# Kernel tuning notes

Hardware: AMD Instinct MI355X
Metric: run time of the kernel (lower is better)

The kernel has to match this reference:

```python
import jax, jax.numpy as jnp
import numpy as np

B, S, D = 2, 1024, 1024
H = 4 * D          # SwiGLU hidden
E = 8              # routed experts
K = 2              # top_k
NS = 1             # shared experts


def setup_inputs() -> dict:
    key = jax.random.key(0)
    ks = jax.random.split(key, 8)
    sc = 0.02  # init scale for stability
    return {
        "x": jax.random.normal(ks[0], (B, S, D), jnp.float32),
        "shared_w1": jax.random.normal(ks[1], (NS, D, H), jnp.float32) * sc,
        "shared_w2": jax.random.normal(ks[2], (NS, D, H), jnp.float32) * sc,
        "shared_w3": jax.random.normal(ks[3], (NS, H, D), jnp.float32) * sc,
        "w1": jax.random.normal(ks[4], (E, D, H), jnp.float32) * sc,
        "w2": jax.random.normal(ks[5], (E, D, H), jnp.float32) * sc,
        "w3": jax.random.normal(ks[6], (E, H, D), jnp.float32) * sc,
        "router_w": jax.random.normal(ks[7], (E, D), jnp.float32) * sc,
    }


def _experts(xf, W1, W2, W3):
    # xf: [T, D]; W1,W2: [E, D, H]; W3: [E, H, D] -> [E, T, D]
    h = jax.nn.silu(jnp.einsum("td,edh->eth", xf, W1)) * jnp.einsum("td,edh->eth", xf, W2)
    return jnp.einsum("eth,ehd->etd", h, W3)


def reference(x, shared_w1, shared_w2, shared_w3, w1, w2, w3, router_w):
    b, s, d = x.shape
    xf = x.reshape(-1, d)                       # [T, D]
    T = xf.shape[0]

    # shared experts (summed over NS experts)
    shared_out = _experts(xf, shared_w1, shared_w2, shared_w3).sum(axis=0)  # [T, D]

    # router: nn.Linear(dim, E, bias=False) => x @ W^T
    logits = jnp.einsum("td,ed->te", xf, router_w)   # [T, E]
    probs = jax.nn.softmax(logits, axis=1)
    topw, topi = jax.lax.top_k(probs, K)             # [T, K]
    topw = topw / topw.sum(axis=-1, keepdims=True)

    # dense combine-weight matrix [T, E]: zero except at selected experts
    cw = jnp.zeros((T, E), x.dtype).at[jnp.arange(T)[:, None], topi].add(topw)

    # all-expert outputs, weighted combine (faithful to masked loop + scatter-add)
    y = _experts(xf, w1, w2, w3)                     # [E, T, D]
    routed = jnp.einsum("te,etd->td", cw, y)         # [T, D]

    out = (shared_out + routed).reshape(b, s, d)
    return (out, logits)
```

## Files before the change

### kernel.cpp

```cpp
#include <hip/hip_runtime.h>


#define TD 2048
#define DD 1024
#define HH 4096
#define NEXP 8

typedef _Float16 f16x8 __attribute__((ext_vector_type(8)));
typedef _Float16 f16x4 __attribute__((ext_vector_type(4)));
typedef float f32x4 __attribute__((ext_vector_type(4)));

#define WS_COUNTS   0
#define WS_CURS     64
#define WS_HBASE    128
#define WS_TOKLIST  256
#define WS_TOPI     65792
#define WS_TOPW     82176
#define WS_POS      98560
#define WS_XH       131072
#define WS_H        4325376
#define WS_WT       63045632
#define WTSLOT      ((size_t)DD * HH)

typedef __attribute__((address_space(3))) void lds_void;
typedef const __attribute__((address_space(1))) void gbl_void;
__device__ __forceinline__ void gld16(void* l, const void* g) {
  __builtin_amdgcn_global_load_lds((gbl_void*)g, (lds_void*)l, 16, 0, 0);
}

__device__ __forceinline__ f16x8 frag_ld(const _Float16* tile, int r, int qsel) {
  int q = qsel ^ ((r >> 1) & 3);
  return *(const f16x8*)((const char*)tile + r * 64 + q * 16);
}

__global__ __launch_bounds__(256) void k_xh(const float* __restrict__ x, _Float16* __restrict__ xh) {
  int i = (blockIdx.x * 256 + threadIdx.x) * 8;
  float4 a = *(const float4*)(x + i), b = *(const float4*)(x + i + 4);
  f16x8 v = {(_Float16)a.x, (_Float16)a.y, (_Float16)a.z, (_Float16)a.w,
             (_Float16)b.x, (_Float16)b.y, (_Float16)b.z, (_Float16)b.w};
  *(f16x8*)(xh + i) = v;
}

__global__ __launch_bounds__(256) void k_router(const float* __restrict__ x,
    const float* __restrict__ rw, float* __restrict__ logits,
    int* __restrict__ topi, float* __restrict__ topw, int* __restrict__ counts) {
  int wv = threadIdx.x >> 6, lane = threadIdx.x & 63;
  int t = blockIdx.x * 4 + wv;
  const float* xt = x + (size_t)t * DD;
  float lg[NEXP];
#pragma unroll
  for (int e = 0; e < NEXP; ++e) {
    const float* we = rw + e * DD;
    float acc = 0.f;
#pragma unroll
    for (int j = 0; j < DD / 64; ++j) acc += xt[j * 64 + lane] * we[j * 64 + lane];
#pragma unroll
    for (int off = 32; off; off >>= 1) acc += __shfl_xor(acc, off);
    lg[e] = acc;
  }
  if (lane == 0) {
    float m = lg[0];
#pragma unroll
    for (int e = 1; e < NEXP; ++e) m = fmaxf(m, lg[e]);
    float p[NEXP];
#pragma unroll
    for (int e = 0; e < NEXP; ++e) p[e] = __expf(lg[e] - m);
    int i0 = 0; float p0 = p[0];
#pragma unroll
    for (int e = 1; e < NEXP; ++e) if (p[e] > p0) { p0 = p[e]; i0 = e; }
    int i1 = -1; float p1 = -1.f;
#pragma unroll
    for (int e = 0; e < NEXP; ++e) if (e != i0 && p[e] > p1) { p1 = p[e]; i1 = e; }
    float wsum = p0 + p1;
#pragma unroll
    for (int e = 0; e < NEXP; ++e) logits[t * NEXP + e] = lg[e];
    topi[t * 2] = i0; topi[t * 2 + 1] = i1;
    topw[t * 2] = p0 / wsum; topw[t * 2 + 1] = p1 / wsum;
    atomicAdd(&counts[i0], 1); atomicAdd(&counts[i1], 1);
  }
}

__global__ void k_offsets(const int* __restrict__ counts, int* __restrict__ hbase) {
  if (threadIdx.x == 0) {
    int base = TD;
    for (int e = 0; e < NEXP; ++e) { hbase[e] = base; base += (counts[e] + 127) & ~127; }
  }
}

__global__ void k_scatter(const int* __restrict__ topi, int* __restrict__ curs,
                          int* __restrict__ tokl, int* __restrict__ posarr) {
  int tid = blockIdx.x * 256 + threadIdx.x;
  if (tid >= TD * 2) return;
  int e = topi[tid];
  int pos = atomicAdd(&curs[e], 1);
  tokl[e * TD + pos] = tid >> 1;
  posarr[tid] = pos;
}

__device__ __forceinline__ void transpose_tile(const float* __restrict__ src,
    _Float16* __restrict__ dst, int R, int C, int r0, int c0) {
  __shared__ _Float16 tile[64][68];
  int t = threadIdx.x;
#pragma unroll
  for (int i = 0; i < 4; ++i) {
    int r = (t >> 4) + i * 16;
    int c = (t & 15) * 4;
    float4 v = *(const float4*)(src + (size_t)(r0 + r) * C + c0 + c);
    *(f16x4*)&tile[r][c] = (f16x4){(_Float16)v.x, (_Float16)v.y, (_Float16)v.z, (_Float16)v.w};
  }
  __syncthreads();
#pragma unroll
  for (int i = 0; i < 2; ++i) {
    int cc = (t >> 3) + i * 32;
    int rr = (t & 7) * 8;
    f16x8 hv;
#pragma unroll
    for (int j = 0; j < 8; ++j) hv[j] = tile[rr + j][cc];
    *(f16x8*)(dst + (size_t)(c0 + cc) * R + r0 + rr) = hv;
  }
}

__global__ __launch_bounds__(256) void k_tr1(const float* __restrict__ sw1, const float* __restrict__ sw2,
    const float* __restrict__ w1, const float* __restrict__ w2, _Float16* __restrict__ wt) {
  int id = blockIdx.y;
  const float* src = (id == 0) ? sw1 : (id == 1) ? sw2
                   : (id < 10) ? w1 + (size_t)(id - 2) * DD * HH
                               : w2 + (size_t)(id - 10) * DD * HH;
  _Float16* dst = wt + (size_t)id * WTSLOT;
  transpose_tile(src, dst, DD, HH, (blockIdx.x >> 6) * 64, (blockIdx.x & 63) * 64);
}

__global__ __launch_bounds__(256) void k_tr2(const float* __restrict__ sw3,
    const float* __restrict__ w3, _Float16* __restrict__ wt) {
  int id = blockIdx.y;
  const float* src = (id == 0) ? sw3 : w3 + (size_t)(id - 1) * HH * DD;
  _Float16* dst = wt + (size_t)id * WTSLOT;
  transpose_tile(src, dst, HH, DD, (blockIdx.x >> 4) * 64, (blockIdx.x & 15) * 64);
}

__global__ __launch_bounds__(256, 2) void k_gemm1(
    const _Float16* __restrict__ xh, const _Float16* __restrict__ wt,
    const int* __restrict__ counts, const int* __restrict__ hbase,
    const int* __restrict__ tok_list, _Float16* __restrict__ h) {
  __shared__ _Float16 lA[128 * 32];
  __shared__ _Float16 lB1[128 * 32];
  __shared__ _Float16 lB2[128 * 32];
  __shared__ int stok[128];

  int slot = blockIdx.y;
  const _Float16 *w1t, *w2t;
  int hrow0;
  if (slot < 16) {
    w1t = wt; w2t = wt + WTSLOT; hrow0 = slot * 128;
  } else {
    int e = (slot - 16) >> 4, rt = (slot - 16) & 15;
    if (rt * 128 >= counts[e]) return;
    w1t = wt + (size_t)(2 + e) * WTSLOT;
    w2t = wt + (size_t)(10 + e) * WTSLOT;
    hrow0 = hbase[e] + rt * 128;
  }
  if (threadIdx.x < 128) {
    int tok = (slot < 16) ? (hrow0 + threadIdx.x)
                          : tok_list[((slot - 16) >> 4) * TD + ((slot - 16) & 15) * 128 + threadIdx.x];
    stok[threadIdx.x] = tok;
  }
  __syncthreads();

  int n0 = blockIdx.x * 128;
  int wv = threadIdx.x >> 6, lane = threadIdx.x & 63;
  int wm = (wv & 1) * 64, wn = (wv >> 1) * 64;
  int qsel = lane >> 4;

  const _Float16 *gA[2], *gB1[2], *gB2[2];
  int ldsoff[2];
#pragma unroll
  for (int jj = 0; jj < 2; ++jj) {
    int j = wv * 2 + jj;
    int n = j * 16 + (lane >> 2);
    int q = (lane & 3) ^ ((n >> 1) & 3);
    gA[jj]  = xh + (size_t)stok[n] * DD + q * 8;
    gB1[jj] = w1t + (size_t)(n0 + n) * DD + q * 8;
    gB2[jj] = w2t + (size_t)(n0 + n) * DD + q * 8;
    ldsoff[jj] = j * 1024 + lane * 16;
  }

  f32x4 acc1[4][4] = {}; f32x4 acc2[4][4] = {};

  for (int kk = 0; kk < DD; kk += 32) {
    __syncthreads();
#pragma unroll
    for (int jj = 0; jj < 2; ++jj) {
      gld16((char*)lA + ldsoff[jj], gA[jj] + kk);
      gld16((char*)lB1 + ldsoff[jj], gB1[jj] + kk);
      gld16((char*)lB2 + ldsoff[jj], gB2[jj] + kk);
    }
    __syncthreads();
    f16x8 af[4];
#pragma unroll
    for (int mi = 0; mi < 4; ++mi) af[mi] = frag_ld(lA, wm + mi * 16 + (lane & 15), qsel);
#pragma unroll
    for (int ni = 0; ni < 4; ++ni) {
      f16x8 b1 = frag_ld(lB1, wn + ni * 16 + (lane & 15), qsel);
      f16x8 b2 = frag_ld(lB2, wn + ni * 16 + (lane & 15), qsel);
#pragma unroll
      for (int mi = 0; mi < 4; ++mi) {
        acc1[mi][ni] = __builtin_amdgcn_mfma_f32_16x16x32_f16(af[mi], b1, acc1[mi][ni], 0, 0, 0);
        acc2[mi][ni] = __builtin_amdgcn_mfma_f32_16x16x32_f16(af[mi], b2, acc2[mi][ni], 0, 0, 0);
      }
    }
  }
#pragma unroll
  for (int mi = 0; mi < 4; ++mi)
#pragma unroll
    for (int ni = 0; ni < 4; ++ni)
#pragma unroll
      for (int i = 0; i < 4; ++i) {
        int r = wm + mi * 16 + (lane >> 4) * 4 + i;
        int c = wn + ni * 16 + (lane & 15);
        float a = acc1[mi][ni][i], b = acc2[mi][ni][i];
        h[(size_t)(hrow0 + r) * HH + n0 + c] = (_Float16)((a / (1.f + __expf(-a))) * b);
      }
}

__global__ __launch_bounds__(256, 2) void k_gemm2(
    const _Float16* __restrict__ h, const _Float16* __restrict__ wt,
    const int* __restrict__ counts, const int* __restrict__ hbase,
    _Float16* __restrict__ y0, _Float16* __restrict__ y1) {
  __shared__ _Float16 lA[128 * 32];
  __shared__ _Float16 lB[128 * 32];

  int slot = blockIdx.y;
  const _Float16* w3t;
  int hrow0;
  if (slot < 16) {
    w3t = wt; hrow0 = slot * 128;
  } else {
    int e = (slot - 16) >> 4, rt = (slot - 16) & 15;
    if (rt * 128 >= counts[e]) return;
    w3t = wt + (size_t)(1 + e) * WTSLOT;
    hrow0 = hbase[e] + rt * 128;
  }
  _Float16* y = blockIdx.z ? y1 : y0;
  int kz0 = blockIdx.z * (HH / 2);

  int n0 = blockIdx.x * 128;
  int wv = threadIdx.x >> 6, lane = threadIdx.x & 63;
  int wm = (wv & 1) * 64, wn = (wv >> 1) * 64;
  int qsel = lane >> 4;

  const _Float16 *gA[2], *gB[2];
  int ldsoff[2];
#pragma unroll
  for (int jj = 0; jj < 2; ++jj) {
    int j = wv * 2 + jj;
    int n = j * 16 + (lane >> 2);
    int q = (lane & 3) ^ ((n >> 1) & 3);
    gA[jj] = h   + (size_t)(hrow0 + n) * HH + kz0 + q * 8;
    gB[jj] = w3t + (size_t)(n0 + n)   * HH + kz0 + q * 8;
    ldsoff[jj] = j * 1024 + lane * 16;
  }

  f32x4 acc[4][4] = {};
  for (int kk = 0; kk < HH / 2; kk += 32) {
    __syncthreads();
#pragma unroll
    for (int jj = 0; jj < 2; ++jj) {
      gld16((char*)lA + ldsoff[jj], gA[jj] + kk);
      gld16((char*)lB + ldsoff[jj], gB[jj] + kk);
    }
    __syncthreads();
    f16x8 af[4];
#pragma unroll
    for (int mi = 0; mi < 4; ++mi) af[mi] = frag_ld(lA, wm + mi * 16 + (lane & 15), qsel);
#pragma unroll
    for (int ni = 0; ni < 4; ++ni) {
      f16x8 bf = frag_ld(lB, wn + ni * 16 + (lane & 15), qsel);
#pragma unroll
      for (int mi = 0; mi < 4; ++mi)
        acc[mi][ni] = __builtin_amdgcn_mfma_f32_16x16x32_f16(af[mi], bf, acc[mi][ni], 0, 0, 0);
    }
  }
#pragma unroll
  for (int mi = 0; mi < 4; ++mi)
#pragma unroll
    for (int ni = 0; ni < 4; ++ni)
#pragma unroll
      for (int i = 0; i < 4; ++i) {
        int r = wm + mi * 16 + (lane >> 4) * 4 + i;
        int c = wn + ni * 16 + (lane & 15);
        y[(size_t)(hrow0 + r) * DD + n0 + c] = (_Float16)acc[mi][ni][i];
      }
}

__global__ __launch_bounds__(256) void k_combine(
    const _Float16* __restrict__ y0, const _Float16* __restrict__ y1,
    const int* __restrict__ topi, const float* __restrict__ topw,
    const int* __restrict__ posarr, const int* __restrict__ hbase,
    float* __restrict__ out) {
  int t = blockIdx.x;
  int c = threadIdx.x * 4;
  int e0 = topi[2 * t], e1 = topi[2 * t + 1];
  float w0 = topw[2 * t], w1 = topw[2 * t + 1];
  size_t rs = (size_t)t * DD + c;
  size_t r0 = (size_t)(hbase[e0] + posarr[2 * t]) * DD + c;
  size_t r1 = (size_t)(hbase[e1] + posarr[2 * t + 1]) * DD + c;
  f16x4 s0 = *(const f16x4*)(y0 + rs), s1 = *(const f16x4*)(y1 + rs);
  f16x4 a0 = *(const f16x4*)(y0 + r0), a1 = *(const f16x4*)(y1 + r0);
  f16x4 b0 = *(const f16x4*)(y0 + r1), b1 = *(const f16x4*)(y1 + r1);
  float4 o;
  float* op = &o.x;
#pragma unroll
  for (int i = 0; i < 4; ++i)
    op[i] = (float)s0[i] + (float)s1[i] + w0 * ((float)a0[i] + (float)a1[i])
          + w1 * ((float)b0[i] + (float)b1[i]);
  *(float4*)(out + rs) = o;
}

extern "C" void kernel_launch(void* const* d_in, const int* in_sizes, int n_in,
                              void* d_out, int out_size, void* d_ws, size_t ws_size,
                              hipStream_t stream) {
  const float* x   = (const float*)d_in[0];
  const float* sw1 = (const float*)d_in[1];
  const float* sw2 = (const float*)d_in[2];
  const float* sw3 = (const float*)d_in[3];
  const float* w1  = (const float*)d_in[4];
  const float* w2  = (const float*)d_in[5];
  const float* w3  = (const float*)d_in[6];
  const float* rw  = (const float*)d_in[7];
  float* out = (float*)d_out;
  char* ws = (char*)d_ws;

  int*   counts = (int*)(ws + WS_COUNTS);
  int*   curs   = (int*)(ws + WS_CURS);
  int*   hbase  = (int*)(ws + WS_HBASE);
  int*   tokl   = (int*)(ws + WS_TOKLIST);
  int*   topi   = (int*)(ws + WS_TOPI);
  float* topw   = (float*)(ws + WS_TOPW);
  int*   posarr = (int*)(ws + WS_POS);
  _Float16* xh   = (_Float16*)(ws + WS_XH);
  _Float16* hbuf = (_Float16*)(ws + WS_H);
  _Float16* wt   = (_Float16*)(ws + WS_WT);
  _Float16* ybuf0 = wt + 9 * WTSLOT;
  _Float16* ybuf1 = wt + 11 * WTSLOT;

  hipMemsetAsync(ws, 0, 65792, stream);

  k_xh<<<TD * DD / 2048, 256, 0, stream>>>(x, xh);
  k_router<<<TD / 4, 256, 0, stream>>>(x, rw, out + (size_t)TD * DD, topi, topw, counts);
  k_offsets<<<1, 64, 0, stream>>>(counts, hbase);
  k_scatter<<<16, 256, 0, stream>>>(topi, curs, tokl, posarr);

  k_tr1<<<dim3(1024, 18), 256, 0, stream>>>(sw1, sw2, w1, w2, wt);
  k_gemm1<<<dim3(HH / 128, 144), 256, 0, stream>>>(xh, wt, counts, hbase, tokl, hbuf);
  k_tr2<<<dim3(1024, 9), 256, 0, stream>>>(sw3, w3, wt);
  k_gemm2<<<dim3(DD / 128, 144, 2), 256, 0, stream>>>(hbuf, wt, counts, hbase, ybuf0, ybuf1);
  k_combine<<<TD, 256, 0, stream>>>(ybuf0, ybuf1, topi, topw, posarr, hbase, out);
}
```

Baseline: 791.3 us.

## Double-buffer LDS in expert GEMMs and enlarge weight transpose tiles

Both expert GEMM kernels now use two LDS buffers. The next K-slice is issued into the idle buffer while MFMAs run on the current one, which leaves one barrier per iteration instead of two and hides global-load latency behind compute. The weight transpose kernels now handle 128x64 tiles per block with half as many blocks, so each thread does more work. The cost is twice the LDS per GEMM block, which may limit occupancy, plus a larger transpose tile in shared memory.

Measured after the change: 818.5 us. 3.4% more time.

```diff
diff --git a/kernel.cpp b/kernel.cpp
--- a/kernel.cpp
+++ b/kernel.cpp
@@ -99,10 +99,10 @@
 
 __device__ __forceinline__ void transpose_tile(const float* __restrict__ src,
     _Float16* __restrict__ dst, int R, int C, int r0, int c0) {
-  __shared__ _Float16 tile[64][68];
+  __shared__ _Float16 tile[128][68];
   int t = threadIdx.x;
 #pragma unroll
-  for (int i = 0; i < 4; ++i) {
+  for (int i = 0; i < 8; ++i) {
     int r = (t >> 4) + i * 16;
     int c = (t & 15) * 4;
     float4 v = *(const float4*)(src + (size_t)(r0 + r) * C + c0 + c);
@@ -110,9 +110,9 @@
   }
   __syncthreads();
 #pragma unroll
-  for (int i = 0; i < 2; ++i) {
-    int cc = (t >> 3) + i * 32;
-    int rr = (t & 7) * 8;
+  for (int i = 0; i < 4; ++i) {
+    int cc = (t >> 4) + i * 16;
+    int rr = (t & 15) * 8;
     f16x8 hv;
 #pragma unroll
     for (int j = 0; j < 8; ++j) hv[j] = tile[rr + j][cc];
@@ -127,7 +127,7 @@
                    : (id < 10) ? w1 + (size_t)(id - 2) * DD * HH
                                : w2 + (size_t)(id - 10) * DD * HH;
   _Float16* dst = wt + (size_t)id * WTSLOT;
-  transpose_tile(src, dst, DD, HH, (blockIdx.x >> 6) * 64, (blockIdx.x & 63) * 64);
+  transpose_tile(src, dst, DD, HH, (blockIdx.x >> 6) * 128, (blockIdx.x & 63) * 64);
 }
 
 __global__ __launch_bounds__(256) void k_tr2(const float* __restrict__ sw3,
@@ -135,16 +135,16 @@
   int id = blockIdx.y;
   const float* src = (id == 0) ? sw3 : w3 + (size_t)(id - 1) * HH * DD;
   _Float16* dst = wt + (size_t)id * WTSLOT;
-  transpose_tile(src, dst, HH, DD, (blockIdx.x >> 4) * 64, (blockIdx.x & 15) * 64);
+  transpose_tile(src, dst, HH, DD, (blockIdx.x >> 4) * 128, (blockIdx.x & 15) * 64);
 }
 
 __global__ __launch_bounds__(256, 2) void k_gemm1(
     const _Float16* __restrict__ xh, const _Float16* __restrict__ wt,
     const int* __restrict__ counts, const int* __restrict__ hbase,
     const int* __restrict__ tok_list, _Float16* __restrict__ h) {
-  __shared__ _Float16 lA[128 * 32];
-  __shared__ _Float16 lB1[128 * 32];
-  __shared__ _Float16 lB2[128 * 32];
+  __shared__ _Float16 lA[2][128 * 32];
+  __shared__ _Float16 lB1[2][128 * 32];
+  __shared__ _Float16 lB2[2][128 * 32];
   __shared__ int stok[128];
 
   int slot = blockIdx.y;
@@ -170,6 +170,7 @@
   int wv = threadIdx.x >> 6, lane = threadIdx.x & 63;
   int wm = (wv & 1) * 64, wn = (wv >> 1) * 64;
   int qsel = lane >> 4;
+  int r15 = lane & 15;
 
   const _Float16 *gA[2], *gB1[2], *gB2[2];
   int ldsoff[2];
@@ -184,31 +185,46 @@
     ldsoff[jj] = j * 1024 + lane * 16;
   }
 
+#pragma unroll
+  for (int jj = 0; jj < 2; ++jj) {
+    gld16((char*)lA[0] + ldsoff[jj], gA[jj]);
+    gld16((char*)lB1[0] + ldsoff[jj], gB1[jj]);
+    gld16((char*)lB2[0] + ldsoff[jj], gB2[jj]);
+  }
+
   f32x4 acc1[4][4] = {}; f32x4 acc2[4][4] = {};
 
-  for (int kk = 0; kk < DD; kk += 32) {
-    __syncthreads();
-#pragma unroll
-    for (int jj = 0; jj < 2; ++jj) {
-      gld16((char*)lA + ldsoff[jj], gA[jj] + kk);
-      gld16((char*)lB1 + ldsoff[jj], gB1[jj] + kk);
-      gld16((char*)lB2 + ldsoff[jj], gB2[jj] + kk);
-    }
-    __syncthreads();
+  auto compute = [&](int b) {
     f16x8 af[4];
 #pragma unroll
-    for (int mi = 0; mi < 4; ++mi) af[mi] = frag_ld(lA, wm + mi * 16 + (lane & 15), qsel);
+    for (int mi = 0; mi < 4; ++mi) af[mi] = frag_ld(lA[b], wm + mi * 16 + r15, qsel);
 #pragma unroll
     for (int ni = 0; ni < 4; ++ni) {
-      f16x8 b1 = frag_ld(lB1, wn + ni * 16 + (lane & 15), qsel);
-      f16x8 b2 = frag_ld(lB2, wn + ni * 16 + (lane & 15), qsel);
+      f16x8 b1 = frag_ld(lB1[b], wn + ni * 16 + r15, qsel);
+      f16x8 b2 = frag_ld(lB2[b], wn + ni * 16 + r15, qsel);
 #pragma unroll
       for (int mi = 0; mi < 4; ++mi) {
         acc1[mi][ni] = __builtin_amdgcn_mfma_f32_16x16x32_f16(af[mi], b1, acc1[mi][ni], 0, 0, 0);
         acc2[mi][ni] = __builtin_amdgcn_mfma_f32_16x16x32_f16(af[mi], b2, acc2[mi][ni], 0, 0, 0);
       }
     }
-  }
+  };
+
+  int cur = 0;
+  __syncthreads();
+  for (int kk = 32; kk < DD; kk += 32) {
+#pragma unroll
+    for (int jj = 0; jj < 2; ++jj) {
+      gld16((char*)lA[cur ^ 1] + ldsoff[jj], gA[jj] + kk);
+      gld16((char*)lB1[cur ^ 1] + ldsoff[jj], gB1[jj] + kk);
+      gld16((char*)lB2[cur ^ 1] + ldsoff[jj], gB2[jj] + kk);
+    }
+    compute(cur);
+    __syncthreads();
+    cur ^= 1;
+  }
+  compute(cur);
+
 #pragma unroll
   for (int mi = 0; mi < 4; ++mi)
 #pragma unroll
@@ -226,8 +242,8 @@
     const _Float16* __restrict__ h, const _Float16* __restrict__ wt,
     const int* __restrict__ counts, const int* __restrict__ hbase,
     _Float16* __restrict__ y0, _Float16* __restrict__ y1) {
-  __shared__ _Float16 lA[128 * 32];
-  __shared__ _Float16 lB[128 * 32];
+  __shared__ _Float16 lA[2][128 * 32];
+  __shared__ _Float16 lB[2][128 * 32];
 
   int slot = blockIdx.y;
   const _Float16* w3t;
@@ -247,6 +263,7 @@
   int wv = threadIdx.x >> 6, lane = threadIdx.x & 63;
   int wm = (wv & 1) * 64, wn = (wv >> 1) * 64;
   int qsel = lane >> 4;
+  int r15 = lane & 15;
 
   const _Float16 *gA[2], *gB[2];
   int ldsoff[2];
@@ -260,26 +277,41 @@
     ldsoff[jj] = j * 1024 + lane * 16;
   }
 
+#pragma unroll
+  for (int jj = 0; jj < 2; ++jj) {
+    gld16((char*)lA[0] + ldsoff[jj], gA[jj]);
+    gld16((char*)lB[0] + ldsoff[jj], gB[jj]);
+  }
+
   f32x4 acc[4][4] = {};
-  for (int kk = 0; kk < HH / 2; kk += 32) {
-    __syncthreads();
-#pragma unroll
-    for (int jj = 0; jj < 2; ++jj) {
-      gld16((char*)lA + ldsoff[jj], gA[jj] + kk);
-      gld16((char*)lB + ldsoff[jj], gB[jj] + kk);
-    }
-    __syncthreads();
+
+  auto compute = [&](int b) {
     f16x8 af[4];
 #pragma unroll
-    for (int mi = 0; mi < 4; ++mi) af[mi] = frag_ld(lA, wm + mi * 16 + (lane & 15), qsel);
+    for (int mi = 0; mi < 4; ++mi) af[mi] = frag_ld(lA[b], wm + mi * 16 + r15, qsel);
 #pragma unroll
     for (int ni = 0; ni < 4; ++ni) {
-      f16x8 bf = frag_ld(lB, wn + ni * 16 + (lane & 15), qsel);
+      f16x8 bf = frag_ld(lB[b], wn + ni * 16 + r15, qsel);
 #pragma unroll
       for (int mi = 0; mi < 4; ++mi)
         acc[mi][ni] = __builtin_amdgcn_mfma_f32_16x16x32_f16(af[mi], bf, acc[mi][ni], 0, 0, 0);
     }
-  }
+  };
+
+  int cur = 0;
+  __syncthreads();
+  for (int kk = 32; kk < HH / 2; kk += 32) {
+#pragma unroll
+    for (int jj = 0; jj < 2; ++jj) {
+      gld16((char*)lA[cur ^ 1] + ldsoff[jj], gA[jj] + kk);
+      gld16((char*)lB[cur ^ 1] + ldsoff[jj], gB[jj] + kk);
+    }
+    compute(cur);
+    __syncthreads();
+    cur ^= 1;
+  }
+  compute(cur);
+
 #pragma unroll
   for (int mi = 0; mi < 4; ++mi)
 #pragma unroll
@@ -350,9 +382,9 @@
   k_offsets<<<1, 64, 0, stream>>>(counts, hbase);
   k_scatter<<<16, 256, 0, stream>>>(topi, curs, tokl, posarr);
 
-  k_tr1<<<dim3(1024, 18), 256, 0, stream>>>(sw1, sw2, w1, w2, wt);
+  k_tr1<<<dim3(512, 18), 256, 0, stream>>>(sw1, sw2, w1, w2, wt);
   k_gemm1<<<dim3(HH / 128, 144), 256, 0, stream>>>(xh, wt, counts, hbase, tokl, hbuf);
-  k_tr2<<<dim3(1024, 9), 256, 0, stream>>>(sw3, w3, wt);
+  k_tr2<<<dim3(512, 9), 256, 0, stream>>>(sw3, w3, wt);
   k_gemm2<<<dim3(DD / 128, 144, 2), 256, 0, stream>>>(hbuf, wt, counts, hbase, ybuf0, ybuf1);
   k_combine<<<TD, 256, 0, stream>>>(ybuf0, ybuf1, topi, topw, posarr, hbase, out);
 }
```
